# Performance work log

Hardware: AMD Instinct MI355X
Metric: run time of the kernel (lower is better)

The kernel has to match this reference:

```python
import jax, jax.numpy as jnp
import numpy as np

B, D, P = 1024, 1024, 16  # batch, latent_dim(=out_dim), part_dim

def setup_inputs() -> dict:
    key = jax.random.key(0)
    k1, k2 = jax.random.split(key)
    x = jax.random.normal(k1, (B, D, P), dtype=jnp.float32)
    # per-part Linear weights, torch Linear weight shape [out, in] stacked over parts
    W = jax.random.normal(k2, (P, D, D), dtype=jnp.float32) * 0.02
    return {"x": x, "W": W}

def reference(x, W):
    # x: [B, D, P]; W: [P, O, D] (O == D here). stack_dim=-1: slice last dim,
    # apply part-specific Linear (no bias) + exact GELU, stack on last dim.
    y = jnp.einsum('bdp,pod->bop', x, W)  # grouped per-part GEMM -> [B, O, P]
    return jax.nn.gelu(y, approximate=False)
```

## Files before the change

kernel.cpp:

```cpp
#include <hip/hip_runtime.h>
#include <hip/hip_bf16.h>
#include <math.h>

typedef __hip_bfloat16 bf16;
typedef __attribute__((ext_vector_type(8))) short bf16x8;
typedef __attribute__((ext_vector_type(4))) float f32x4;

#define DI static __device__ __forceinline__

constexpr int NB = 1024;
constexpr int ND = 1024;
constexpr int NP = 16;
constexpr int BK = 32;

DI float gelu_exact(float x) {
    return 0.5f * x * (1.0f + erff(x * 0.70710678118654752f));
}

__global__ __launch_bounds__(256) void pack_x_kernel(const float* __restrict__ x,
                                                     bf16* __restrict__ xp) {
    const int b = blockIdx.x;
    const int t = threadIdx.x;
    const int p = t & 15;
    const int dg = t >> 4;
    const float* xb = x + (size_t)b * ND * NP;
    bf16* dst = xp + (size_t)p * NB * ND + (size_t)b * ND;
#pragma unroll
    for (int c = 0; c < 8; ++c) {
        const int d0 = dg * 64 + c * 8;
        alignas(16) bf16 tmp[8];
#pragma unroll
        for (int j = 0; j < 8; ++j)
            tmp[j] = __float2bfloat16(xb[(size_t)(d0 + j) * NP + p]);
        *reinterpret_cast<bf16x8*>(&dst[d0]) = *reinterpret_cast<const bf16x8*>(tmp);
    }
}

__global__ __launch_bounds__(256) void pack_w_kernel(const float* __restrict__ w,
                                                     bf16* __restrict__ wp) {
    const size_t i = ((size_t)blockIdx.x * 256 + threadIdx.x) * 8;
    const float4 f0 = *reinterpret_cast<const float4*>(&w[i]);
    const float4 f1 = *reinterpret_cast<const float4*>(&w[i + 4]);
    alignas(16) bf16 tmp[8] = { __float2bfloat16(f0.x), __float2bfloat16(f0.y),
                                __float2bfloat16(f0.z), __float2bfloat16(f0.w),
                                __float2bfloat16(f1.x), __float2bfloat16(f1.y),
                                __float2bfloat16(f1.z), __float2bfloat16(f1.w) };
    *reinterpret_cast<bf16x8*>(&wp[i]) = *reinterpret_cast<const bf16x8*>(tmp);
}

template<bool YBF>
__global__ __launch_bounds__(256, 4) void gemm_kernel(const bf16* __restrict__ xp,
                                                      const bf16* __restrict__ wp,
                                                      void* __restrict__ yout) {
    __shared__ bf16 As[2][128 * BK];
    __shared__ bf16 Bs[2][128 * BK];
    const int i = blockIdx.x;
    const int p    = ((i & 7) << 1) | ((i >> 9) & 1);
    const int tile = (i >> 3) & 63;
    const int ot = (tile & 7) * 128;
    const int bt = (tile >> 3) * 128;
    const bf16* A  = xp + (size_t)p * NB * ND;
    const bf16* Bm = wp + (size_t)p * ND * ND;
    const int t = threadIdx.x;
    const int l = t & 63;
    const int w = t >> 6;
    const int wr = w >> 1, wc = w & 1;

    f32x4 acc[4][4] = {};

    auto stage = [&](int buf, int k0) {
#pragma unroll
        for (int r = 0; r < 2; ++r) {
            const int c   = r * 256 + t;
            const int row = c >> 2;
            const int cc  = c & 3;
            const bf16* ga = A  + (size_t)(bt + row) * ND + (k0 + cc * 8);
            const bf16* gb = Bm + (size_t)(ot + row) * ND + (k0 + cc * 8);
            bf16* la = &As[buf][(r * 256 + w * 64) * 8];
            bf16* lb = &Bs[buf][(r * 256 + w * 64) * 8];
            __builtin_amdgcn_global_load_lds((const __attribute__((address_space(1))) void*)ga,
                                             (__attribute__((address_space(3))) void*)la, 16, 0, 0);
            __builtin_amdgcn_global_load_lds((const __attribute__((address_space(1))) void*)gb,
                                             (__attribute__((address_space(3))) void*)lb, 16, 0, 0);
        }
    };

    int buf = 0;
    stage(0, 0);
    const int NK = ND / BK;
    for (int kt = 0; kt < NK; ++kt) {
        __syncthreads();
        if (kt + 1 < NK) stage(buf ^ 1, (kt + 1) * BK);
        const int lr = l & 15;
        const int lk = (l >> 4) * 8;
        bf16x8 af[4], bf_[4];
#pragma unroll
        for (int m = 0; m < 4; ++m)
            af[m] = *reinterpret_cast<const bf16x8*>(&As[buf][(wr * 64 + m * 16 + lr) * BK + lk]);
#pragma unroll
        for (int n = 0; n < 4; ++n)
            bf_[n] = *reinterpret_cast<const bf16x8*>(&Bs[buf][(wc * 64 + n * 16 + lr) * BK + lk]);
#pragma unroll
        for (int m = 0; m < 4; ++m)
#pragma unroll
            for (int n = 0; n < 4; ++n)
                acc[m][n] = __builtin_amdgcn_mfma_f32_16x16x32_bf16(af[m], bf_[n], acc[m][n], 0, 0, 0);
        buf ^= 1;
    }

    const int lr4 = (l >> 4) * 4;
    const int lc  = l & 15;
    const int row0 = bt + wr * 64, col0 = ot + wc * 64;
#pragma unroll
    for (int m = 0; m < 4; ++m) {
#pragma unroll
        for (int j = 0; j < 4; ++j) {
            const int r = row0 + m * 16 + lr4 + j;
#pragma unroll
            for (int n = 0; n < 4; ++n) {
                const int c = col0 + n * 16 + lc;
                const float v = gelu_exact(acc[m][n][j]);
                if (YBF) {
                    ((bf16*)yout)[(size_t)p * NB * ND + (size_t)r * ND + c] =
                        __float2bfloat16(v);
                } else {
                    ((float*)yout)[((size_t)r * ND + c) * NP + p] = v;
                }
            }
        }
    }
}

__global__ __launch_bounds__(256) void unpack_kernel(const bf16* __restrict__ y,
                                                     float* __restrict__ out) {
    const size_t f = (size_t)blockIdx.x * 256 + threadIdx.x;
    const int    p0 = (int)(f & 3) * 4;
    const size_t o  = (f >> 2) & 1023;
    const size_t b  = f >> 12;
    const bf16* yb = y + b * (size_t)ND + o;
    float4 v;
    v.x = __bfloat162float(yb[(size_t)(p0 + 0) * (NB * ND)]);
    v.y = __bfloat162float(yb[(size_t)(p0 + 1) * (NB * ND)]);
    v.z = __bfloat162float(yb[(size_t)(p0 + 2) * (NB * ND)]);
    v.w = __bfloat162float(yb[(size_t)(p0 + 3) * (NB * ND)]);
    reinterpret_cast<float4*>(out)[f] = v;
}

__global__ __launch_bounds__(256) void fallback_kernel(const float* __restrict__ x,
                                                       const float* __restrict__ w,
                                                       float* __restrict__ out) {
    __shared__ float As[64][17];
    __shared__ float Bs[64][17];
    const int p = blockIdx.z, bt = blockIdx.y * 64, ot = blockIdx.x * 64;
    const int t = threadIdx.x;
    const int tx = t & 15, ty = t >> 4;
    float acc[4][4] = {};
    for (int k0 = 0; k0 < ND; k0 += 16) {
        __syncthreads();
#pragma unroll
        for (int i = 0; i < 4; ++i) {
            const int idx = i * 256 + t;
            const int r = idx >> 4, k = idx & 15;
            As[r][k] = x[((size_t)(bt + r) * ND + k0 + k) * NP + p];
            Bs[r][k] = w[(size_t)p * ND * ND + (size_t)(ot + r) * ND + k0 + k];
        }
        __syncthreads();
#pragma unroll
        for (int k = 0; k < 16; ++k) {
            float a[4], bb[4];
#pragma unroll
            for (int i = 0; i < 4; ++i) a[i] = As[ty * 4 + i][k];
#pragma unroll
            for (int j = 0; j < 4; ++j) bb[j] = Bs[tx * 4 + j][k];
#pragma unroll
            for (int i = 0; i < 4; ++i)
#pragma unroll
                for (int j = 0; j < 4; ++j) acc[i][j] += a[i] * bb[j];
        }
    }
#pragma unroll
    for (int i = 0; i < 4; ++i)
#pragma unroll
        for (int j = 0; j < 4; ++j)
            out[((size_t)(bt + ty * 4 + i) * ND + (ot + tx * 4 + j)) * NP + p] =
                gelu_exact(acc[i][j]);
}

extern "C" void kernel_launch(void* const* d_in, const int* in_sizes, int n_in,
                              void* d_out, int out_size, void* d_ws, size_t ws_size,
                              hipStream_t stream) {
    const float* x = (const float*)d_in[0];
    const float* w = (const float*)d_in[1];
    float* out = (float*)d_out;

    const size_t nElem     = (size_t)NP * NB * ND;
    const size_t packBytes = nElem * sizeof(bf16) * 2;
    const size_t yBytes    = nElem * sizeof(bf16);

    if (ws_size >= packBytes) {
        bf16* xp = (bf16*)d_ws;
        bf16* wp = xp + nElem;
        pack_x_kernel<<<NB, 256, 0, stream>>>(x, xp);
        pack_w_kernel<<<(int)(nElem / (256 * 8)), 256, 0, stream>>>(w, wp);
        if (ws_size >= packBytes + yBytes) {
            bf16* y = (bf16*)((char*)d_ws + packBytes);
            gemm_kernel<true><<<1024, 256, 0, stream>>>(xp, wp, y);
            unpack_kernel<<<(int)(nElem / (256 * 4)), 256, 0, stream>>>(y, out);
        } else {
            gemm_kernel<false><<<1024, 256, 0, stream>>>(xp, wp, out);
        }
    } else {
        fallback_kernel<<<dim3(16, 16, 16), 256, 0, stream>>>(x, w, out);
    }
}
```

Before: 122.3 us.

## Use 256x256 tile GEMM with triple-buffered LDS, swizzle, and fused pack kernel

Replaces the 128x128 grouped GEMM with a 512-thread 256x256-tile kernel. It triple-buffers LDS via async global-to-LDS loads, uses an XOR swizzle to avoid bank conflicts, and splits the k-step into two halves that interleave staging with MFMA under explicit waitcnt, barriers and priority hints. The two pack kernels are merged into one launch. This should raise data reuse and overlap loads with compute. The trade-off is fewer blocks (256 over the CUs) and more registers per thread.

Measured after the change: 119.4 us. -2.4%, faster.

```diff
diff --git a/kernel.cpp b/kernel.cpp
--- a/kernel.cpp
+++ b/kernel.cpp
@@ -11,47 +11,170 @@
 constexpr int NB = 1024;
 constexpr int ND = 1024;
 constexpr int NP = 16;
-constexpr int BK = 32;
+constexpr int BKT = 32;
+constexpr int NKT = ND / BKT;
 
 DI float gelu_exact(float x) {
     return 0.5f * x * (1.0f + erff(x * 0.70710678118654752f));
 }
 
-__global__ __launch_bounds__(256) void pack_x_kernel(const float* __restrict__ x,
-                                                     bf16* __restrict__ xp) {
-    const int b = blockIdx.x;
+__global__ __launch_bounds__(256) void pack_kernel(const float* __restrict__ x,
+                                                   const float* __restrict__ w,
+                                                   bf16* __restrict__ xp,
+                                                   bf16* __restrict__ wp) {
+    if (blockIdx.x < NB) {
+        const int b = blockIdx.x;
+        const int t = threadIdx.x;
+        const int p = t & 15;
+        const int dg = t >> 4;
+        const float* xb = x + (size_t)b * ND * NP;
+        bf16* dst = xp + (size_t)p * NB * ND + (size_t)b * ND;
+#pragma unroll
+        for (int c = 0; c < 8; ++c) {
+            const int d0 = dg * 64 + c * 8;
+            alignas(16) bf16 tmp[8];
+#pragma unroll
+            for (int j = 0; j < 8; ++j)
+                tmp[j] = __float2bfloat16(xb[(size_t)(d0 + j) * NP + p]);
+            *reinterpret_cast<bf16x8*>(&dst[d0]) = *reinterpret_cast<const bf16x8*>(tmp);
+        }
+    } else {
+        const size_t i = ((size_t)(blockIdx.x - NB) * 256 + threadIdx.x) * 8;
+        const float4 f0 = *reinterpret_cast<const float4*>(&w[i]);
+        const float4 f1 = *reinterpret_cast<const float4*>(&w[i + 4]);
+        alignas(16) bf16 tmp[8] = { __float2bfloat16(f0.x), __float2bfloat16(f0.y),
+                                    __float2bfloat16(f0.z), __float2bfloat16(f0.w),
+                                    __float2bfloat16(f1.x), __float2bfloat16(f1.y),
+                                    __float2bfloat16(f1.z), __float2bfloat16(f1.w) };
+        *reinterpret_cast<bf16x8*>(&wp[i]) = *reinterpret_cast<const bf16x8*>(tmp);
+    }
+}
+
+__global__ __launch_bounds__(512, 2) void gemm8_kernel(const bf16* __restrict__ xp,
+                                                       const bf16* __restrict__ wp,
+                                                       bf16* __restrict__ y) {
+    __shared__ bf16 As[3][256 * BKT];
+    __shared__ bf16 Bs[3][256 * BKT];
+    const int i = blockIdx.x;
+    const int p    = ((i & 7) << 1) | ((i >> 3) & 1);
+    const int tile = i >> 4;
+    const int bt = (tile >> 2) * 256;
+    const int ot = (tile & 3) * 256;
+    const bf16* A  = xp + (size_t)p * NB * ND;
+    const bf16* Bm = wp + (size_t)p * ND * ND;
     const int t = threadIdx.x;
-    const int p = t & 15;
-    const int dg = t >> 4;
-    const float* xb = x + (size_t)b * ND * NP;
-    bf16* dst = xp + (size_t)p * NB * ND + (size_t)b * ND;
-#pragma unroll
-    for (int c = 0; c < 8; ++c) {
-        const int d0 = dg * 64 + c * 8;
-        alignas(16) bf16 tmp[8];
-#pragma unroll
-        for (int j = 0; j < 8; ++j)
-            tmp[j] = __float2bfloat16(xb[(size_t)(d0 + j) * NP + p]);
-        *reinterpret_cast<bf16x8*>(&dst[d0]) = *reinterpret_cast<const bf16x8*>(tmp);
-    }
-}
-
-__global__ __launch_bounds__(256) void pack_w_kernel(const float* __restrict__ w,
-                                                     bf16* __restrict__ wp) {
-    const size_t i = ((size_t)blockIdx.x * 256 + threadIdx.x) * 8;
-    const float4 f0 = *reinterpret_cast<const float4*>(&w[i]);
-    const float4 f1 = *reinterpret_cast<const float4*>(&w[i + 4]);
-    alignas(16) bf16 tmp[8] = { __float2bfloat16(f0.x), __float2bfloat16(f0.y),
-                                __float2bfloat16(f0.z), __float2bfloat16(f0.w),
-                                __float2bfloat16(f1.x), __float2bfloat16(f1.y),
-                                __float2bfloat16(f1.z), __float2bfloat16(f1.w) };
-    *reinterpret_cast<bf16x8*>(&wp[i]) = *reinterpret_cast<const bf16x8*>(tmp);
-}
-
-template<bool YBF>
-__global__ __launch_bounds__(256, 4) void gemm_kernel(const bf16* __restrict__ xp,
-                                                      const bf16* __restrict__ wp,
-                                                      void* __restrict__ yout) {
+    const int l = t & 63, w = t >> 6;
+    const int wr = w >> 2, wc = w & 3;
+    const int lr = l & 15, g = l >> 4;
+
+    f32x4 acc[8][4] = {};
+
+    auto stage = [&](int buf, int kt, int q) {
+        const int s   = ((q & 1) * 8 + w) * 64 + l;
+        const int row = s >> 2;
+        const int cb  = (s & 3) ^ (row & 3);
+        const bf16* gsrc = (q < 2 ? A + (size_t)(bt + row) * ND
+                                  : Bm + (size_t)(ot + row) * ND) + kt * BKT + cb * 8;
+        bf16* ldst = (q < 2 ? &As[buf][((q & 1) * 8 + w) * 512]
+                            : &Bs[buf][((q & 1) * 8 + w) * 512]);
+        __builtin_amdgcn_global_load_lds((const __attribute__((address_space(1))) void*)gsrc,
+                                         (__attribute__((address_space(3))) void*)ldst, 16, 0, 0);
+    };
+    auto readA = [&](int buf, int m) -> bf16x8 {
+        const int row  = wr * 128 + m * 16 + lr;
+        const int slot = row * 4 + (g ^ (row & 3));
+        return *reinterpret_cast<const bf16x8*>(&As[buf][slot * 8]);
+    };
+    auto readB = [&](int buf, int n) -> bf16x8 {
+        const int row  = wc * 64 + n * 16 + lr;
+        const int slot = row * 4 + (g ^ (row & 3));
+        return *reinterpret_cast<const bf16x8*>(&Bs[buf][slot * 8]);
+    };
+
+#pragma unroll
+    for (int q = 0; q < 4; ++q) stage(0, 0, q);
+#pragma unroll
+    for (int q = 0; q < 4; ++q) stage(1, 1, q);
+    asm volatile("s_waitcnt vmcnt(4)" ::: "memory");
+    __builtin_amdgcn_s_barrier();
+    __builtin_amdgcn_sched_barrier(0);
+
+    int bufc = 0, bufs = 2;
+#pragma unroll 1
+    for (int kt = 0; kt < NKT; ++kt) {
+        bf16x8 bfr[4], af[4];
+#pragma unroll
+        for (int n = 0; n < 4; ++n) bfr[n] = readB(bufc, n);
+#pragma unroll
+        for (int m = 0; m < 4; ++m) af[m] = readA(bufc, m);
+        if (kt + 2 < NKT) { stage(bufs, kt + 2, 0); stage(bufs, kt + 2, 1); }
+        __builtin_amdgcn_s_barrier();
+        asm volatile("s_waitcnt lgkmcnt(0)" ::: "memory");
+        __builtin_amdgcn_s_setprio(1);
+#pragma unroll
+        for (int m = 0; m < 4; ++m)
+#pragma unroll
+            for (int n = 0; n < 4; ++n)
+                acc[m][n] = __builtin_amdgcn_mfma_f32_16x16x32_bf16(af[m], bfr[n], acc[m][n], 0, 0, 0);
+        __builtin_amdgcn_s_setprio(0);
+        __builtin_amdgcn_s_barrier();
+#pragma unroll
+        for (int m = 0; m < 4; ++m) af[m] = readA(bufc, 4 + m);
+        if (kt + 2 < NKT) { stage(bufs, kt + 2, 2); stage(bufs, kt + 2, 3); }
+        __builtin_amdgcn_s_barrier();
+        asm volatile("s_waitcnt lgkmcnt(0)" ::: "memory");
+        __builtin_amdgcn_s_setprio(1);
+#pragma unroll
+        for (int m = 0; m < 4; ++m)
+#pragma unroll
+            for (int n = 0; n < 4; ++n)
+                acc[4 + m][n] = __builtin_amdgcn_mfma_f32_16x16x32_bf16(af[m], bfr[n], acc[4 + m][n], 0, 0, 0);
+        __builtin_amdgcn_s_setprio(0);
+        if (kt < NKT - 1) {
+            if (kt + 2 < NKT) asm volatile("s_waitcnt vmcnt(4)" ::: "memory");
+            else              asm volatile("s_waitcnt vmcnt(0)" ::: "memory");
+            __builtin_amdgcn_s_barrier();
+            __builtin_amdgcn_sched_barrier(0);
+        }
+        bufc = (bufc == 2) ? 0 : bufc + 1;
+        bufs = (bufs == 2) ? 0 : bufs + 1;
+    }
+
+    const int r4 = (l >> 4) * 4, lc = l & 15;
+    bf16* yp = y + (size_t)p * NB * ND;
+#pragma unroll
+    for (int m = 0; m < 8; ++m) {
+#pragma unroll
+        for (int j = 0; j < 4; ++j) {
+            const int row = bt + wr * 128 + m * 16 + r4 + j;
+#pragma unroll
+            for (int n = 0; n < 4; ++n) {
+                const int col = ot + wc * 64 + n * 16 + lc;
+                yp[(size_t)row * ND + col] = __float2bfloat16(gelu_exact(acc[m][n][j]));
+            }
+        }
+    }
+}
+
+__global__ __launch_bounds__(256) void unpack_kernel(const bf16* __restrict__ y,
+                                                     float* __restrict__ out) {
+    const size_t f = (size_t)blockIdx.x * 256 + threadIdx.x;
+    const int    p0 = (int)(f & 3) * 4;
+    const size_t o  = (f >> 2) & 1023;
+    const size_t b  = f >> 12;
+    const bf16* yb = y + b * (size_t)ND + o;
+    float4 v;
+    v.x = __bfloat162float(yb[(size_t)(p0 + 0) * (NB * ND)]);
+    v.y = __bfloat162float(yb[(size_t)(p0 + 1) * (NB * ND)]);
+    v.z = __bfloat162float(yb[(size_t)(p0 + 2) * (NB * ND)]);
+    v.w = __bfloat162float(yb[(size_t)(p0 + 3) * (NB * ND)]);
+    reinterpret_cast<float4*>(out)[f] = v;
+}
+
+__global__ __launch_bounds__(256, 4) void gemm_direct_kernel(const bf16* __restrict__ xp,
+                                                             const bf16* __restrict__ wp,
+                                                             float* __restrict__ out) {
+    constexpr int BK = 32;
     __shared__ bf16 As[2][128 * BK];
     __shared__ bf16 Bs[2][128 * BK];
     const int i = blockIdx.x;
@@ -65,9 +188,7 @@
     const int l = t & 63;
     const int w = t >> 6;
     const int wr = w >> 1, wc = w & 1;
-
     f32x4 acc[4][4] = {};
-
     auto stage = [&](int buf, int k0) {
 #pragma unroll
         for (int r = 0; r < 2; ++r) {
@@ -84,66 +205,41 @@
                                              (__attribute__((address_space(3))) void*)lb, 16, 0, 0);
         }
     };
-
     int buf = 0;
     stage(0, 0);
-    const int NK = ND / BK;
-    for (int kt = 0; kt < NK; ++kt) {
+    for (int kt = 0; kt < ND / BK; ++kt) {
         __syncthreads();
-        if (kt + 1 < NK) stage(buf ^ 1, (kt + 1) * BK);
+        if (kt + 1 < ND / BK) stage(buf ^ 1, (kt + 1) * BK);
         const int lr = l & 15;
         const int lk = (l >> 4) * 8;
-        bf16x8 af[4], bf_[4];
+        bf16x8 af[4], bfr[4];
 #pragma unroll
         for (int m = 0; m < 4; ++m)
             af[m] = *reinterpret_cast<const bf16x8*>(&As[buf][(wr * 64 + m * 16 + lr) * BK + lk]);
 #pragma unroll
         for (int n = 0; n < 4; ++n)
-            bf_[n] = *reinterpret_cast<const bf16x8*>(&Bs[buf][(wc * 64 + n * 16 + lr) * BK + lk]);
+            bfr[n] = *reinterpret_cast<const bf16x8*>(&Bs[buf][(wc * 64 + n * 16 + lr) * BK + lk]);
 #pragma unroll
         for (int m = 0; m < 4; ++m)
 #pragma unroll
             for (int n = 0; n < 4; ++n)
-                acc[m][n] = __builtin_amdgcn_mfma_f32_16x16x32_bf16(af[m], bf_[n], acc[m][n], 0, 0, 0);
+                acc[m][n] = __builtin_amdgcn_mfma_f32_16x16x32_bf16(af[m], bfr[n], acc[m][n], 0, 0, 0);
         buf ^= 1;
     }
-
     const int lr4 = (l >> 4) * 4;
     const int lc  = l & 15;
     const int row0 = bt + wr * 64, col0 = ot + wc * 64;
 #pragma unroll
-    for (int m = 0; m < 4; ++m) {
+    for (int m = 0; m < 4; ++m)
 #pragma unroll
         for (int j = 0; j < 4; ++j) {
             const int r = row0 + m * 16 + lr4 + j;
 #pragma unroll
             for (int n = 0; n < 4; ++n) {
                 const int c = col0 + n * 16 + lc;
-                const float v = gelu_exact(acc[m][n][j]);
-                if (YBF) {
-                    ((bf16*)yout)[(size_t)p * NB * ND + (size_t)r * ND + c] =
-                        __float2bfloat16(v);
-                } else {
-                    ((float*)yout)[((size_t)r * ND + c) * NP + p] = v;
-                }
+                out[((size_t)r * ND + c) * NP + p] = gelu_exact(acc[m][n][j]);
             }
         }
-    }
-}
-
-__global__ __launch_bounds__(256) void unpack_kernel(const bf16* __restrict__ y,
-                                                     float* __restrict__ out) {
-    const size_t f = (size_t)blockIdx.x * 256 + threadIdx.x;
-    const int    p0 = (int)(f & 3) * 4;
-    const size_t o  = (f >> 2) & 1023;
-    const size_t b  = f >> 12;
-    const bf16* yb = y + b * (size_t)ND + o;
-    float4 v;
-    v.x = __bfloat162float(yb[(size_t)(p0 + 0) * (NB * ND)]);
-    v.y = __bfloat162float(yb[(size_t)(p0 + 1) * (NB * ND)]);
-    v.z = __bfloat162float(yb[(size_t)(p0 + 2) * (NB * ND)]);
-    v.w = __bfloat162float(yb[(size_t)(p0 + 3) * (NB * ND)]);
-    reinterpret_cast<float4*>(out)[f] = v;
 }
 
 __global__ __launch_bounds__(256) void fallback_kernel(const float* __restrict__ x,
@@ -200,14 +296,13 @@
     if (ws_size >= packBytes) {
         bf16* xp = (bf16*)d_ws;
         bf16* wp = xp + nElem;
-        pack_x_kernel<<<NB, 256, 0, stream>>>(x, xp);
-        pack_w_kernel<<<(int)(nElem / (256 * 8)), 256, 0, stream>>>(w, wp);
+        pack_kernel<<<NB + (int)(nElem / (256 * 8)), 256, 0, stream>>>(x, w, xp, wp);
         if (ws_size >= packBytes + yBytes) {
             bf16* y = (bf16*)((char*)d_ws + packBytes);
-            gemm_kernel<true><<<1024, 256, 0, stream>>>(xp, wp, y);
+            gemm8_kernel<<<256, 512, 0, stream>>>(xp, wp, y);
             unpack_kernel<<<(int)(nElem / (256 * 4)), 256, 0, stream>>>(y, out);
         } else {
-            gemm_kernel<false><<<1024, 256, 0, stream>>>(xp, wp, out);
+            gemm_direct_kernel<<<1024, 256, 0, stream>>>(xp, wp, out);
         }
     } else {
         fallback_kernel<<<dim3(16, 16, 16), 256, 0, stream>>>(x, w, out);
```
